# Performance work log

Hardware: AMD Instinct MI355X
Metric: run time of the kernel (lower is better)

## Reference

```python
import jax, jax.numpy as jnp
import numpy as np

QMAX = 255.0  # bit=8 unsigned activation range


def ste_round(x):
    # straight-through round: exact integer rounding in fwd, identity grad
    return x + jax.lax.stop_gradient(jnp.round(x) - x)


def conv3x3(x, w, stride=1):
    return jax.lax.conv_general_dilated(
        x, w, window_strides=(stride, stride), padding=((1, 1), (1, 1)),
        dimension_numbers=('NCHW', 'OIHW', 'NCHW'))


def setup_inputs() -> dict:
    key = jax.random.key(0)
    k0, k1, k2 = jax.random.split(key, 3)
    N, C, H, W = 64, 256, 28, 28
    # uint8 activations and int8 (symmetric) weights, stored as integer-valued fp32
    x = jax.random.randint(k0, (N, C, H, W), 0, 256).astype(jnp.float32)
    w1 = jax.random.randint(k1, (C, C, 3, 3), -128, 128).astype(jnp.float32)
    w2 = jax.random.randint(k2, (C, C, 3, 3), -128, 128).astype(jnp.float32)
    f = jnp.float32
    return dict(
        x=x, w1=w1, w2=w2,
        s_x=f(0.05), z_x=f(128.0),
        s_w1=f(0.01), s_conv1=f(0.08), z_conv1=f(120.0),
        s_w2=f(0.01), s_conv2=f(0.07), z_conv2=f(130.0),
        s_add=f(0.09), z_add=f(125.0))


def qconv(x_q, w_q, s_in, z_in, s_w, s_out, z_out, stride=1):
    # integer-arithmetic conv: sum((x - z_in) * w) then requantize
    acc = conv3x3(x_q - z_in, w_q, stride)
    M = s_in * s_w / s_out  # per-cluster requant multiplier (cluster 0)
    return jnp.clip(ste_round(M * acc) + z_out, 0.0, QMAX)


def qadd(a, s_a, z_a, b, s_b, z_b, s_out, z_out):
    # fused dequant of both branches + residual add + requant
    y = (s_a / s_out) * (a - z_a) + (s_b / s_out) * (b - z_b)
    return jnp.clip(ste_round(y) + z_out, 0.0, QMAX)


def reference(x, w1, w2, s_x, z_x, s_w1, s_conv1, z_conv1,
              s_w2, s_conv2, z_conv2, s_add, z_add):
    out = qconv(x, w1, s_x, z_x, s_w1, s_conv1, z_conv1)          # conv1
    out = qconv(out, w2, s_conv1, z_conv1, s_w2, s_conv2, z_conv2)  # conv2
    return qadd(x, s_x, z_x, out, s_conv2, z_conv2, s_add, z_add)   # shortcut
```

## Files before the change

kernel.cpp:

```cpp
#include <hip/hip_runtime.h>
#include <stdint.h>

#define HWP 784
#define NPOS 50176
#define PLN ((size_t)NPOS * 64)
#define PAD_OFF 31232

typedef int   int4v   __attribute__((ext_vector_type(4)));
typedef int   int16v  __attribute__((ext_vector_type(16)));
typedef float float4v __attribute__((ext_vector_type(4)));
using as1_cv = const __attribute__((address_space(1))) void;
using as3_v  = __attribute__((address_space(3))) void;

__global__ __launch_bounds__(256) void k_nhwc(const float* __restrict__ x,
                                              int8_t* __restrict__ x8) {
    __shared__ int lA[256 * 15];
    __shared__ __align__(16) int lB[56 * 68];
    const int tid = threadIdx.x;
    const int P0 = blockIdx.x * 56;
    const int n = P0 / HWP;
    const int hw0 = P0 % HWP;
    const float* xb = x + (size_t)n * 256 * HWP + hw0;
#pragma unroll
    for (int k = 0; k < 14; ++k) {
        int e = tid + k * 256;
        int c = e / 14, pq = e % 14;
        float4v v = *(const float4v*)(xb + (size_t)c * HWP + pq * 4);
        int b0 = ((int)v[0] - 128) & 255;
        int b1 = ((int)v[1] - 128) & 255;
        int b2 = ((int)v[2] - 128) & 255;
        int b3 = ((int)v[3] - 128) & 255;
        lA[c * 15 + pq] = b0 | (b1 << 8) | (b2 << 16) | (b3 << 24);
    }
    __syncthreads();
#pragma unroll
    for (int k = 0; k < 4; ++k) {
        int u = tid + k * 256;
        if (u < 896) {
            int cg = u / 14, pq = u % 14;
            int d0 = lA[(cg * 4 + 0) * 15 + pq];
            int d1 = lA[(cg * 4 + 1) * 15 + pq];
            int d2 = lA[(cg * 4 + 2) * 15 + pq];
            int d3 = lA[(cg * 4 + 3) * 15 + pq];
#pragma unroll
            for (int j = 0; j < 4; ++j) {
                int sh = j * 8;
                int o = ((d0 >> sh) & 255) | (((d1 >> sh) & 255) << 8)
                      | (((d2 >> sh) & 255) << 16) | (((d3 >> sh) & 255) << 24);
                lB[(pq * 4 + j) * 68 + cg] = o;
            }
        }
    }
    __syncthreads();
#pragma unroll
    for (int k = 0; k < 4; ++k) {
        int ch = tid + k * 256;
        if (ch < 896) {
            int g = ch / 224, rem = ch % 224;
            int pos = rem >> 2, c4 = rem & 3;
            int4v val = *(const int4v*)&lB[pos * 68 + g * 16 + c4 * 4];
            *(int4v*)(x8 + (size_t)g * PLN + (size_t)(P0 + pos) * 64 + c4 * 16) = val;
        }
    }
}

__global__ __launch_bounds__(256) void k_w_prep(const float* __restrict__ wa,
                                                const float* __restrict__ wb,
                                                int8_t* __restrict__ w8a,
                                                int8_t* __restrict__ w8b,
                                                int* __restrict__ wsa,
                                                int* __restrict__ wsb) {
    __shared__ int red[256];
    const int which = blockIdx.x >> 8;
    const int oc = blockIdx.x & 255;
    const float* w = which ? wb : wa;
    int8_t* w8 = which ? w8b : w8a;
    int* wsum = which ? wsb : wsa;
    const int t = threadIdx.x;
    const float* src = w + (size_t)oc * 2304 + (size_t)t * 9;
    const int g = oc >> 5;
    const int l = ((t >> 4) & 1) * 32 + (oc & 31);
    const int j = t & 15;
    const int s2 = (t >> 5) & 1;
    const int kb = t >> 6;
    int acc = 0;
#pragma unroll
    for (int tap = 0; tap < 9; ++tap) {
        int wv = (int)src[tap];
        acc += wv;
        int oo = ((((tap * 4 + kb) * 2 + s2) * 8 + g) * 64 + l) * 16 + j;
        w8[oo] = (int8_t)wv;
    }
    red[t] = acc;
    __syncthreads();
    for (int st = 128; st > 0; st >>= 1) {
        if (t < st) red[t] += red[t + st];
        __syncthreads();
    }
    if (t == 0) wsum[oc] = red[0];
}

template<bool FUSED>
__global__ __launch_bounds__(256, 4) void k_qconv_t(const int8_t* __restrict__ in8,
        const int8_t* __restrict__ w8, const int* __restrict__ wsum,
        const float* __restrict__ s_in_p, const float* __restrict__ s_w_p,
        const float* __restrict__ s_out_p, const float* __restrict__ z_in_p,
        const float* __restrict__ z_out_p, int8_t* __restrict__ out8,
        const int8_t* __restrict__ x8, const float* __restrict__ sxp,
        const float* __restrict__ zxp, const float* __restrict__ sap,
        const float* __restrict__ zap, float* __restrict__ outf) {
    __shared__ __align__(16) int8_t slab[33280];
    const int tid = threadIdx.x;
    const int lane = tid & 63;
    const int half = lane >> 5;
    const int wv = tid >> 6;
    const int p0 = blockIdx.x * 64;

#pragma unroll
    for (int k = 0; k < 8; ++k) {
        int chunkid = tid + k * 256;
        if (chunkid < 1952) {
            int q = chunkid >> 4;
            int cs = chunkid & 15;
            int cg = cs ^ (q & 15);
            int qg = p0 - 29 + q;
            qg = qg < 0 ? 0 : (qg > NPOS - 1 ? NPOS - 1 : qg);
            const int8_t* src = in8 + (size_t)(cg >> 2) * PLN
                                    + (size_t)qg * 64 + (cg & 3) * 16;
            __builtin_amdgcn_global_load_lds((as1_cv*)src,
                                             (as3_v*)&slab[chunkid * 16], 16, 0, 0);
        }
    }

    const int zi = (int)z_in_p[0] - 128;
    const int spl = (zi & 0xff) * 0x01010101;
    if (tid < 16) {
        int4v pv; pv[0] = spl; pv[1] = spl; pv[2] = spl; pv[3] = spl;
        *(int4v*)&slab[PAD_OFF + tid * 16] = pv;
    }

    int rowpos[2], ph[2], pw[2];
#pragma unroll
    for (int mt = 0; mt < 2; ++mt) {
        rowpos[mt] = mt * 32 + (lane & 31);
        int p = p0 + rowpos[mt];
        int hw = p % HWP;
        ph[mt] = hw / 28;
        pw[mt] = hw % 28;
    }

    int16v acc[2][2];
#pragma unroll
    for (int mt = 0; mt < 2; ++mt)
#pragma unroll
        for (int nt = 0; nt < 2; ++nt)
#pragma unroll
            for (int r = 0; r < 16; ++r) acc[mt][nt][r] = 0;

    const int8_t* wlane = w8 + wv * 2048 + lane * 16;

    __syncthreads();

#pragma unroll
    for (int u = 0; u < 36; ++u) {
        const int tap = u >> 2, kb = u & 3;
        const int dh = tap / 3 - 1;
        const int dw = tap % 3 - 1;
        const int8_t* wb_ = wlane + (size_t)u * 16384;
        int4v b[2][2];
        b[0][0] = *(const int4v*)(wb_);
        b[1][0] = *(const int4v*)(wb_ + 1024);
        b[0][1] = *(const int4v*)(wb_ + 8192);
        b[1][1] = *(const int4v*)(wb_ + 9216);
        int4v a[2][2];
#pragma unroll
        for (int mt = 0; mt < 2; ++mt) {
            int q = rowpos[mt] + dh * 28 + dw + 29;
            bool ok = ((unsigned)(ph[mt] + dh) < 28u) & ((unsigned)(pw[mt] + dw) < 28u);
            int ab = (ok ? (q << 8) : PAD_OFF) ^ ((q & 15) << 4) ^ (half << 4);
            a[mt][0] = *(const int4v*)&slab[ab ^ ((kb * 4 + 0) << 4)];
            a[mt][1] = *(const int4v*)&slab[ab ^ ((kb * 4 + 2) << 4)];
        }
#pragma unroll
        for (int s = 0; s < 2; ++s)
#pragma unroll
            for (int mt = 0; mt < 2; ++mt)
#pragma unroll
                for (int nt = 0; nt < 2; ++nt)
                    acc[mt][nt] = __builtin_amdgcn_mfma_i32_32x32x32_i8(
                        a[mt][s], b[nt][s], acc[mt][nt], 0, 0, 0);
    }

    const float Mf = s_in_p[0] * s_w_p[0] / s_out_p[0];
    const float zof = z_out_p[0];
    const int zoffi = 128 - (int)z_in_p[0];

    if (!FUSED) {
        __syncthreads();
        int8_t* tpb = slab + wv * 5120;
#pragma unroll
        for (int mt = 0; mt < 2; ++mt)
#pragma unroll
            for (int nt = 0; nt < 2; ++nt) {
                int oc = wv * 64 + nt * 32 + (lane & 31);
                int corr = zoffi * wsum[oc];
#pragma unroll
                for (int r = 0; r < 16; ++r) {
                    int prow = (r & 3) + 8 * (r >> 2) + 4 * half;
                    int pl = mt * 32 + prow;
                    float q = rintf(Mf * (float)(acc[mt][nt][r] + corr)) + zof;
                    q = fminf(fmaxf(q, 0.0f), 255.0f);
                    tpb[pl * 80 + nt * 32 + (lane & 31)] = (int8_t)((int)q - 128);
                }
            }
        int8_t* o8p = out8 + (size_t)wv * PLN + (size_t)(p0 + lane) * 64;
        const int8_t* rowp = tpb + lane * 80;
#pragma unroll
        for (int k = 0; k < 4; ++k)
            *(int4v*)(o8p + k * 16) = *(const int4v*)(rowp + k * 16);
    } else {
        const float ra = sxp[0] / sap[0];
        const float rb = s_out_p[0] / sap[0];
        const float zx = zxp[0];
        const float z2 = z_out_p[0];
        const float za = zap[0];
        __syncthreads();
        float* tp = (float*)slab + wv * 2080;
        const int pl = lane & 31;
#pragma unroll
        for (int mt = 0; mt < 2; ++mt) {
#pragma unroll
            for (int nt = 0; nt < 2; ++nt) {
                int oc = wv * 64 + nt * 32 + (lane & 31);
                int corr = zoffi * wsum[oc];
#pragma unroll
                for (int r = 0; r < 16; ++r) {
                    int prow = (r & 3) + 8 * (r >> 2) + 4 * half;
                    float q2 = rintf(Mf * (float)(acc[mt][nt][r] + corr)) + zof;
                    q2 = fminf(fmaxf(q2, 0.0f), 255.0f);
                    tp[prow * 65 + nt * 32 + (lane & 31)] = q2;
                }
            }
            const int pglob = p0 + mt * 32 + pl;
            const int n = pglob / HWP;
            const int hwo = pglob % HWP;
            const int8_t* x8p = x8 + (size_t)wv * PLN + (size_t)pglob * 64 + half * 32;
            int4v r0 = *(const int4v*)x8p;
            int4v r1 = *(const int4v*)(x8p + 16);
            int xb[8];
            xb[0] = r0[0]; xb[1] = r0[1]; xb[2] = r0[2]; xb[3] = r0[3];
            xb[4] = r1[0]; xb[5] = r1[1]; xb[6] = r1[2]; xb[7] = r1[3];
            float* obase = outf + ((size_t)(n * 256 + wv * 64 + half * 32)) * HWP + hwo;
#pragma unroll
            for (int j = 0; j < 32; ++j) {
                int bv = (xb[j >> 2] >> ((j & 3) * 8)) & 255;
                int xval = (int)(int8_t)bv + 128;
                float q2 = tp[pl * 65 + half * 32 + j];
                float y = ra * ((float)xval - zx) + rb * (q2 - z2);
                float qf = rintf(y) + za;
                qf = fminf(fmaxf(qf, 0.0f), 255.0f);
                obase[(size_t)j * HWP] = qf;
            }
        }
    }
}

extern "C" void kernel_launch(void* const* d_in, const int* in_sizes, int n_in,
                              void* d_out, int out_size, void* d_ws, size_t ws_size,
                              hipStream_t stream) {
    (void)in_sizes; (void)n_in; (void)out_size; (void)ws_size;
    const float* x    = (const float*)d_in[0];
    const float* w1   = (const float*)d_in[1];
    const float* w2   = (const float*)d_in[2];
    const float* s_x  = (const float*)d_in[3];
    const float* z_x  = (const float*)d_in[4];
    const float* s_w1 = (const float*)d_in[5];
    const float* s_c1 = (const float*)d_in[6];
    const float* z_c1 = (const float*)d_in[7];
    const float* s_w2 = (const float*)d_in[8];
    const float* s_c2 = (const float*)d_in[9];
    const float* z_c2 = (const float*)d_in[10];
    const float* s_ad = (const float*)d_in[11];
    const float* z_ad = (const float*)d_in[12];
    float* out = (float*)d_out;

    int8_t* ws    = (int8_t*)d_ws;
    int8_t* x8    = ws;
    int8_t* o1    = ws + 12845056;
    int8_t* w8a   = ws + 25690112;
    int8_t* w8b   = ws + 26279936;
    int*    wsum1 = (int*)(ws + 26869760);
    int*    wsum2 = (int*)(ws + 26870784);

    k_nhwc<<<896, 256, 0, stream>>>(x, x8);
    k_w_prep<<<512, 256, 0, stream>>>(w1, w2, w8a, w8b, wsum1, wsum2);
    k_qconv_t<false><<<784, 256, 0, stream>>>(x8, w8a, wsum1,
        s_x, s_w1, s_c1, z_x, z_c1, o1,
        nullptr, nullptr, nullptr, nullptr, nullptr, nullptr);
    k_qconv_t<true><<<784, 256, 0, stream>>>(o1, w8b, wsum2,
        s_c1, s_w2, s_c2, z_c1, z_c2, nullptr,
        x8, s_x, z_x, s_ad, z_ad, out);
}
```

Before: 212.4 us.

## Stage conv weights through double-buffered LDS with async global-to-LDS loads

Weights are no longer loaded per lane straight from global memory inside the MFMA loop. Each 8 KB weight slice is now copied into a double-buffered LDS region with global_load_lds, prefetching the next slice while the current one is consumed. The loop is split into 72 half-steps with a block barrier after each, and s_setprio is raised around the MFMA group. The LDS footprint grows to about 49 KB and launch bounds drop to 3 blocks per CU, so occupancy and barrier overhead are traded for hiding weight-load latency.

```diff
diff --git a/kernel.cpp b/kernel.cpp
--- a/kernel.cpp
+++ b/kernel.cpp
@@ -5,6 +5,7 @@
 #define NPOS 50176
 #define PLN ((size_t)NPOS * 64)
 #define PAD_OFF 31232
+#define BOFF 33280
 
 typedef int   int4v   __attribute__((ext_vector_type(4)));
 typedef int   int16v  __attribute__((ext_vector_type(16)));
@@ -101,7 +102,7 @@
 }
 
 template<bool FUSED>
-__global__ __launch_bounds__(256, 4) void k_qconv_t(const int8_t* __restrict__ in8,
+__global__ __launch_bounds__(256, 3) void k_qconv_t(const int8_t* __restrict__ in8,
         const int8_t* __restrict__ w8, const int* __restrict__ wsum,
         const float* __restrict__ s_in_p, const float* __restrict__ s_w_p,
         const float* __restrict__ s_out_p, const float* __restrict__ z_in_p,
@@ -109,7 +110,7 @@
         const int8_t* __restrict__ x8, const float* __restrict__ sxp,
         const float* __restrict__ zxp, const float* __restrict__ sap,
         const float* __restrict__ zap, float* __restrict__ outf) {
-    __shared__ __align__(16) int8_t slab[33280];
+    __shared__ __align__(16) int8_t slab[49664];
     const int tid = threadIdx.x;
     const int lane = tid & 63;
     const int half = lane >> 5;
@@ -132,6 +133,14 @@
         }
     }
 
+    {
+        const int8_t* bs = w8 + tid * 16;
+        __builtin_amdgcn_global_load_lds((as1_cv*)bs,
+                                         (as3_v*)&slab[BOFF + tid * 16], 16, 0, 0);
+        __builtin_amdgcn_global_load_lds((as1_cv*)(bs + 4096),
+                                         (as3_v*)&slab[BOFF + 4096 + tid * 16], 16, 0, 0);
+    }
+
     const int zi = (int)z_in_p[0] - 128;
     const int spl = (zi & 0xff) * 0x01010101;
     if (tid < 16) {
@@ -157,38 +166,47 @@
 #pragma unroll
             for (int r = 0; r < 16; ++r) acc[mt][nt][r] = 0;
 
-    const int8_t* wlane = w8 + wv * 2048 + lane * 16;
-
     __syncthreads();
 
 #pragma unroll
-    for (int u = 0; u < 36; ++u) {
+    for (int p = 0; p < 72; ++p) {
+        if (p < 71) {
+            const int8_t* bsrc = w8 + (size_t)(p + 1) * 8192 + tid * 16;
+            int8_t* bdst = slab + BOFF + ((p + 1) & 1) * 8192 + tid * 16;
+            __builtin_amdgcn_global_load_lds((as1_cv*)bsrc, (as3_v*)bdst, 16, 0, 0);
+            __builtin_amdgcn_global_load_lds((as1_cv*)(bsrc + 4096),
+                                             (as3_v*)(bdst + 4096), 16, 0, 0);
+        }
+        const int u = p >> 1, s = p & 1;
         const int tap = u >> 2, kb = u & 3;
         const int dh = tap / 3 - 1;
         const int dw = tap % 3 - 1;
-        const int8_t* wb_ = wlane + (size_t)u * 16384;
-        int4v b[2][2];
-        b[0][0] = *(const int4v*)(wb_);
-        b[1][0] = *(const int4v*)(wb_ + 1024);
-        b[0][1] = *(const int4v*)(wb_ + 8192);
-        b[1][1] = *(const int4v*)(wb_ + 9216);
-        int4v a[2][2];
-#pragma unroll
-        for (int mt = 0; mt < 2; ++mt) {
-            int q = rowpos[mt] + dh * 28 + dw + 29;
-            bool ok = ((unsigned)(ph[mt] + dh) < 28u) & ((unsigned)(pw[mt] + dw) < 28u);
+        const int koff = (kb * 4 + 2 * s) << 4;
+        int4v a0, a1, b0, b1;
+        {
+            int q = rowpos[0] + dh * 28 + dw + 29;
+            bool ok = ((unsigned)(ph[0] + dh) < 28u) & ((unsigned)(pw[0] + dw) < 28u);
             int ab = (ok ? (q << 8) : PAD_OFF) ^ ((q & 15) << 4) ^ (half << 4);
-            a[mt][0] = *(const int4v*)&slab[ab ^ ((kb * 4 + 0) << 4)];
-            a[mt][1] = *(const int4v*)&slab[ab ^ ((kb * 4 + 2) << 4)];
-        }
-#pragma unroll
-        for (int s = 0; s < 2; ++s)
-#pragma unroll
-            for (int mt = 0; mt < 2; ++mt)
-#pragma unroll
-                for (int nt = 0; nt < 2; ++nt)
-                    acc[mt][nt] = __builtin_amdgcn_mfma_i32_32x32x32_i8(
-                        a[mt][s], b[nt][s], acc[mt][nt], 0, 0, 0);
+            a0 = *(const int4v*)&slab[ab ^ koff];
+        }
+        {
+            int q = rowpos[1] + dh * 28 + dw + 29;
+            bool ok = ((unsigned)(ph[1] + dh) < 28u) & ((unsigned)(pw[1] + dw) < 28u);
+            int ab = (ok ? (q << 8) : PAD_OFF) ^ ((q & 15) << 4) ^ (half << 4);
+            a1 = *(const int4v*)&slab[ab ^ koff];
+        }
+        {
+            const int bb = BOFF + (p & 1) * 8192 + wv * 2048 + lane * 16;
+            b0 = *(const int4v*)&slab[bb];
+            b1 = *(const int4v*)&slab[bb + 1024];
+        }
+        __builtin_amdgcn_s_setprio(1);
+        acc[0][0] = __builtin_amdgcn_mfma_i32_32x32x32_i8(a0, b0, acc[0][0], 0, 0, 0);
+        acc[0][1] = __builtin_amdgcn_mfma_i32_32x32x32_i8(a0, b1, acc[0][1], 0, 0, 0);
+        acc[1][0] = __builtin_amdgcn_mfma_i32_32x32x32_i8(a1, b0, acc[1][0], 0, 0, 0);
+        acc[1][1] = __builtin_amdgcn_mfma_i32_32x32x32_i8(a1, b1, acc[1][1], 0, 0, 0);
+        __builtin_amdgcn_s_setprio(0);
+        if (p < 71) __syncthreads();
     }
 
     const float Mf = s_in_p[0] * s_w_p[0] / s_out_p[0];
```

Result: slower. 231.9 us (+9.2%).
